# Optimization experiments

Measured on AMD Instinct MI355X. Metric: run time of the kernel, lower is better.

Reference implementation:

```python
import jax, jax.numpy as jnp
import numpy as np

N_HEAD, N_MIX, D_MODEL, D_K, D_V = 8, 2, 512, 64, 64
BN_EPS = 1e-5


def avg_pool_3x3_s2(x):
    # AvgPool2d(kernel=3, stride=2, pad=1, count_include_pad=False) on NCHW
    win = (1, 1, 3, 3)
    stride = (1, 1, 2, 2)
    pad = [(0, 0), (0, 0), (1, 1), (1, 1)]
    s = jax.lax.reduce_window(x, 0.0, jax.lax.add, win, stride, pad)
    ones = jnp.ones((1, 1, x.shape[2], x.shape[3]), x.dtype)
    cnt = jax.lax.reduce_window(ones, 0.0, jax.lax.add, win, stride, pad)
    return s / cnt


def conv1x1(x, w, b=None):
    # w: [out_c, in_c]; x: [B, in_c, H, W]
    y = jnp.einsum('oc,bchw->bohw', w, x)
    if b is not None:
        y = y + b[None, :, None, None]
    return y


def setup_inputs() -> dict:
    key = jax.random.key(0)
    ks = jax.random.split(key, 8)
    B, H, W = 2, 56, 56
    std_kq = np.sqrt(2.0 / (D_MODEL + D_K)).astype(np.float32)
    std_v = np.sqrt(2.0 / (D_MODEL + D_V)).astype(np.float32)
    std_mix = np.power(N_MIX, -0.5).astype(np.float32)
    return {
        'x': jax.random.normal(ks[0], (B, D_MODEL, H, W), jnp.float32),
        'w_qs': jax.random.normal(ks[1], (N_HEAD * D_K, D_MODEL), jnp.float32) * std_kq,
        'b_qs': jnp.zeros((N_HEAD * D_K,), jnp.float32),
        'w_vs': jax.random.normal(ks[2], (N_HEAD * D_V, D_MODEL), jnp.float32) * std_v,
        'b_vs': jnp.zeros((N_HEAD * D_V,), jnp.float32),
        'mix_w': jax.random.uniform(ks[3], (N_MIX, D_K), jnp.float32, -std_mix, std_mix),
        'w_out': jax.random.normal(ks[4], (D_MODEL, N_HEAD * D_V), jnp.float32) * 0.02,
        'bn_gamma': jnp.ones((D_MODEL,), jnp.float32),
        'bn_beta': jnp.zeros((D_MODEL,), jnp.float32),
    }


def reference(x, w_qs, b_qs, w_vs, b_vs, mix_w, w_out, bn_gamma, bn_beta):
    B, C, H, W = x.shape
    N = H * W
    m = N_MIX
    d = D_K // m  # per-mixture dim
    temperature = D_K ** 0.5

    px = avg_pool_3x3_s2(x)  # [B, C, H/2, W/2]
    N2 = px.shape[2] * px.shape[3]

    # conv_ks aliases conv_qs in the original (shared weights)
    qt = conv1x1(x, w_qs, b_qs).reshape(B * N_HEAD, D_K, N)
    kt = conv1x1(px, w_qs, b_qs).reshape(B * N_HEAD, D_K, N2)
    vt = conv1x1(px, w_vs, b_vs).reshape(B * N_HEAD, D_V, N2)

    # mixture weights pi: softmax over mixtures of weight @ mean_q
    bar_qt = qt.mean(axis=2)  # [B', D_K]
    pi = jax.nn.softmax(jnp.einsum('md,bd->bm', mix_w, bar_qt), axis=1)  # [B', m]

    q = qt.reshape(B * N_HEAD * m, d, N).transpose(0, 2, 1)  # [B'm, N, d]
    k2 = kt.reshape(B * N_HEAD * m, d, N2)  # [B'm, d, N2]

    attn = jnp.einsum('bnd,bdk->bnk', q, k2) / temperature  # [B'm, N, N2]
    attn = jax.nn.softmax(attn, axis=2)
    # dropout is identity in eval mode
    attn = (attn * pi.reshape(-1, 1, 1)).reshape(B * N_HEAD, m, N, N2).sum(1)

    out = jnp.einsum('bnk,bvk->bnv', attn, vt)  # [B', N, D_V]
    out = out.transpose(0, 2, 1).reshape(B, N_HEAD * D_V, H, W)
    out = conv1x1(out, w_out)  # no bias
    # BatchNorm2d in eval mode: running_mean=0, running_var=1
    inv = 1.0 / jnp.sqrt(jnp.float32(1.0 + BN_EPS))
    out = out * inv * bn_gamma[None, :, None, None] + bn_beta[None, :, None, None]
    return out + x
```

## Files before the change

### kernel.cpp

```cpp
#include <hip/hip_runtime.h>
#include <math.h>

typedef unsigned short u16;
typedef short bf16x8 __attribute__((ext_vector_type(8)));
typedef float f32x4 __attribute__((ext_vector_type(4)));

#define MFMA(a, b, c) __builtin_amdgcn_mfma_f32_16x16x32_bf16(a, b, c, 0, 0, 0)

#define SCALE_K 0.18033688011112043f

__device__ __forceinline__ float bf2f(u16 v) {
    union { float f; unsigned u; } x;
    x.u = ((unsigned)v) << 16;
    return x.f;
}
__device__ __forceinline__ u16 f2bf(float f) {
    union { float f; unsigned u; } x;
    x.f = f;
    unsigned r = x.u + 0x7FFF + ((x.u >> 16) & 1);
    return (u16)(r >> 16);
}

__global__ __launch_bounds__(256) void cvt_kernel(const float* __restrict__ s0,
                                                  const float* __restrict__ s1,
                                                  const float* __restrict__ s2,
                                                  u16* __restrict__ d0, u16* __restrict__ d1,
                                                  u16* __restrict__ d2) {
    int i = blockIdx.x * 256 + threadIdx.x;
    const float* s = (blockIdx.y == 0) ? s0 : ((blockIdx.y == 1) ? s1 : s2);
    u16* d = (blockIdx.y == 0) ? d0 : ((blockIdx.y == 1) ? d1 : d2);
    d[i] = f2bf(s[i]);
}

__global__ __launch_bounds__(256) void transpose_kernel(const float* __restrict__ x,
                                                        u16* __restrict__ xT) {
    __shared__ u16 tile[64][65];
    int b = blockIdx.z;
    int n0 = blockIdx.x * 64, c0 = blockIdx.y * 64;
    int j = threadIdx.x & 63, q = threadIdx.x >> 6;
    const float* xb = x + b * 512 * 3136;
#pragma unroll
    for (int it = 0; it < 16; ++it) {
        int r = q * 16 + it;
        tile[r][j] = f2bf(xb[(c0 + r) * 3136 + n0 + j]);
    }
    __syncthreads();
    u16* xTb = xT + b * 3136 * 512;
#pragma unroll
    for (int it = 0; it < 16; ++it) {
        int r = q * 16 + it;
        xTb[(n0 + r) * 512 + c0 + j] = tile[j][r];
    }
}

__global__ __launch_bounds__(256) void pool_kernel(const u16* __restrict__ xT,
                                                   u16* __restrict__ pxT) {
    int n2 = blockIdx.x;
    int b = blockIdx.y;
    int t = threadIdx.x;
    int i = n2 / 28, jj = n2 % 28;
    float s0 = 0.f, s1 = 0.f;
    int cnt = 0;
    const u16* xb = xT + b * 3136 * 512;
#pragma unroll
    for (int dr = 0; dr < 3; dr++) {
        int r = 2 * i - 1 + dr;
        if (r < 0 || r >= 56) continue;
#pragma unroll
        for (int dc = 0; dc < 3; dc++) {
            int cc = 2 * jj - 1 + dc;
            if (cc < 0 || cc >= 56) continue;
            const u16* row = xb + (r * 56 + cc) * 512;
            s0 += bf2f(row[t]);
            s1 += bf2f(row[t + 256]);
            cnt++;
        }
    }
    float invc = 1.0f / (float)cnt;
    u16* op = pxT + (b * 784 + n2) * 512;
    op[t] = f2bf(s0 * invc);
    op[t + 256] = f2bf(s1 * invc);
}

__device__ __forceinline__ void gemm_core(const u16* __restrict__ A, int lda, int M,
                                          const u16* __restrict__ BT, int ldb, int Ncol,
                                          int K, int row0, int col0, f32x4 acc[4][4]) {
    int lane = threadIdx.x & 63;
    int lr = lane & 15, lg = lane >> 4;
    int ar[4], bc[4];
#pragma unroll
    for (int i = 0; i < 4; i++) {
        int r = row0 + i * 16 + lr;
        ar[i] = (r < M) ? r : (M - 1);
    }
#pragma unroll
    for (int j = 0; j < 4; j++) {
        int cj = col0 + j * 16 + lr;
        bc[j] = (cj < Ncol) ? cj : (Ncol - 1);
    }
    for (int k = 0; k < K; k += 32) {
        int ko = k + lg * 8;
        bf16x8 af[4], bfr[4];
#pragma unroll
        for (int i = 0; i < 4; i++) af[i] = *(const bf16x8*)(A + ar[i] * lda + ko);
#pragma unroll
        for (int j = 0; j < 4; j++) bfr[j] = *(const bf16x8*)(BT + bc[j] * ldb + ko);
#pragma unroll
        for (int i = 0; i < 4; i++)
#pragma unroll
            for (int j = 0; j < 4; j++) acc[i][j] = MFMA(af[i], bfr[j], acc[i][j]);
    }
}

__global__ __launch_bounds__(256) void gemm_qk(const u16* __restrict__ xT,
                                               const u16* __restrict__ W,
                                               const float* __restrict__ bias,
                                               u16* __restrict__ out, int M, int Npad,
                                               float oscale) {
    int b = blockIdx.z;
    int w = threadIdx.x >> 6;
    int row0 = blockIdx.y * 128 + (w >> 1) * 64;
    int col0 = blockIdx.x * 128 + (w & 1) * 64;
    f32x4 acc[4][4];
#pragma unroll
    for (int i = 0; i < 4; i++)
#pragma unroll
        for (int j = 0; j < 4; j++) acc[i][j] = (f32x4){0.f, 0.f, 0.f, 0.f};
    gemm_core(xT + b * M * 512, 512, M, W, 512, 512, 512, row0, col0, acc);
    int lane = threadIdx.x & 63;
    int lr = lane & 15, lg = lane >> 4;
#pragma unroll
    for (int j = 0; j < 4; j++) {
        int oc = col0 + j * 16 + lr;
        float bs = bias[oc];
        int bh = b * 8 + (oc >> 6), dk = oc & 63;
        u16* op = out + (bh * Npad) * 64 + dk;
#pragma unroll
        for (int i = 0; i < 4; i++) {
#pragma unroll
            for (int r = 0; r < 4; r++) {
                int n = row0 + i * 16 + lg * 4 + r;
                if (n < M) op[n * 64] = f2bf((acc[i][j][r] + bs) * oscale);
                else if (n < Npad) op[n * 64] = 0;
            }
        }
    }
}

__global__ __launch_bounds__(256) void gemm_v(const u16* __restrict__ W,
                                              const u16* __restrict__ pxT,
                                              const float* __restrict__ bias,
                                              u16* __restrict__ vt) {
    int b = blockIdx.z;
    int w = threadIdx.x >> 6;
    int row0 = blockIdx.y * 128 + (w >> 1) * 64;
    int col0 = blockIdx.x * 128 + (w & 1) * 64;
    f32x4 acc[4][4];
#pragma unroll
    for (int i = 0; i < 4; i++)
#pragma unroll
        for (int j = 0; j < 4; j++) acc[i][j] = (f32x4){0.f, 0.f, 0.f, 0.f};
    gemm_core(W, 512, 512, pxT + b * 784 * 512, 512, 784, 512, row0, col0, acc);
    int lane = threadIdx.x & 63;
    int lr = lane & 15, lg = lane >> 4;
#pragma unroll
    for (int i = 0; i < 4; i++) {
#pragma unroll
        for (int r = 0; r < 4; r++) {
            int oc = row0 + i * 16 + lg * 4 + r;
            float bs = bias[oc];
            u16* vp = vt + ((b * 8 + (oc >> 6)) * 80 + (oc & 63)) * 800;
#pragma unroll
            for (int j = 0; j < 4; j++) {
                int n2 = col0 + j * 16 + lr;
                if (n2 < 784) vp[n2] = f2bf(acc[i][j][r] + bs);
                else if (n2 < 800) vp[n2] = 0;
            }
        }
    }
}

__global__ __launch_bounds__(256) void vpad_kernel(u16* __restrict__ vt) {
    int idx = blockIdx.x * 256 + threadIdx.x;
    int col = idx % 800;
    int row = (idx / 800) & 15;
    int bh = idx / (16 * 800);
    u16 v = (row == 0 && col < 784) ? (u16)0x3F80 : (u16)0;
    vt[(bh * 80 + 64 + row) * 800 + col] = v;
}

__global__ __launch_bounds__(256) void pi_stage1(const u16* __restrict__ qt,
                                                 float* __restrict__ part) {
    __shared__ float red[4][64];
    int chunk = blockIdx.x, bh = blockIdx.y;
    int t = threadIdx.x, dk = t & 63, seg = t >> 6;
    const u16* q = qt + (bh * 3136 + chunk * 112) * 64 + dk;
    float s = 0.f;
    for (int n = seg; n < 112; n += 4) s += bf2f(q[n * 64]);
    red[seg][dk] = s;
    __syncthreads();
    if (t < 64) part[(bh * 28 + chunk) * 64 + t] =
        red[0][t] + red[1][t] + red[2][t] + red[3][t];
}

__global__ __launch_bounds__(64) void pi_stage2(const float* __restrict__ part,
                                                const float* __restrict__ mix_w,
                                                float* __restrict__ pi) {
    int bh = blockIdx.x, lane = threadIdx.x;
    float bar = 0.f;
#pragma unroll
    for (int c = 0; c < 28; c++) bar += part[(bh * 28 + c) * 64 + lane];
    bar *= (1.0f / 3136.0f);
    float l0 = mix_w[lane] * bar;
    float l1 = mix_w[64 + lane] * bar;
#pragma unroll
    for (int d = 1; d < 64; d <<= 1) {
        l0 += __shfl_xor(l0, d);
        l1 += __shfl_xor(l1, d);
    }
    if (lane == 0) {
        float mx = fmaxf(l0, l1);
        float e0 = __expf(l0 - mx), e1 = __expf(l1 - mx);
        float inv = 1.0f / (e0 + e1);
        pi[bh * 2 + 0] = e0 * inv;
        pi[bh * 2 + 1] = e1 * inv;
    }
}

__global__ __launch_bounds__(256) void attn_kernel(const u16* __restrict__ qt,
                                                   const u16* __restrict__ kt,
                                                   const u16* __restrict__ vt,
                                                   const float* __restrict__ pi,
                                                   u16* __restrict__ ao) {
    __shared__ __attribute__((aligned(16))) u16 p_lds[4][2][16][40];
    int w = threadIdx.x >> 6, lane = threadIdx.x & 63;
    int lr = lane & 15, lg = lane >> 4;
    int bh = blockIdx.y;
    int qbase = (blockIdx.x * 4 + w) * 16;
    const u16* qp = qt + (bh * 3136 + qbase) * 64;
    const u16* kp = kt + bh * 800 * 64;
    const u16* vp = vt + bh * 80 * 800;

    bf16x8 qf[2];
    qf[0] = *(const bf16x8*)(qp + lr * 64 + lg * 8);
    qf[1] = *(const bf16x8*)(qp + lr * 64 + 32 + lg * 8);

    f32x4 O[2][4], Osum[2];
#pragma unroll
    for (int m = 0; m < 2; m++) {
#pragma unroll
        for (int t = 0; t < 4; t++) O[m][t] = (f32x4){0.f, 0.f, 0.f, 0.f};
        Osum[m] = (f32x4){0.f, 0.f, 0.f, 0.f};
    }

    for (int c = 0; c < 25; ++c) {
        int base = c * 32;
        bf16x8 vf[4], vfs;
#pragma unroll
        for (int t = 0; t < 4; t++)
            vf[t] = *(const bf16x8*)(vp + (t * 16 + lr) * 800 + base + lg * 8);
        vfs = *(const bf16x8*)(vp + (64 + lr) * 800 + base + lg * 8);
#pragma unroll
        for (int m = 0; m < 2; m++) {
            bf16x8 kf0 = *(const bf16x8*)(kp + (base + lr) * 64 + m * 32 + lg * 8);
            bf16x8 kf1 = *(const bf16x8*)(kp + (base + 16 + lr) * 64 + m * 32 + lg * 8);
            f32x4 s0 = MFMA(qf[m], kf0, ((f32x4){0.f, 0.f, 0.f, 0.f}));
            f32x4 s1 = MFMA(qf[m], kf1, ((f32x4){0.f, 0.f, 0.f, 0.f}));
#pragma unroll
            for (int r = 0; r < 4; r++) {
                float p0 = __builtin_amdgcn_exp2f(s0[r]);
                float p1 = __builtin_amdgcn_exp2f(s1[r]);
                unsigned u;
                asm("v_cvt_pk_bf16_f32 %0, %1, %2" : "=v"(u) : "v"(p0), "v"(p1));
                p_lds[w][m][lg * 4 + r][lr] = (u16)u;
                p_lds[w][m][lg * 4 + r][16 + lr] = (u16)(u >> 16);
            }
        }
#pragma unroll
        for (int m = 0; m < 2; m++) {
            bf16x8 pf = *(const bf16x8*)(&p_lds[w][m][lr][lg * 8]);
#pragma unroll
            for (int t = 0; t < 4; t++) O[m][t] = MFMA(pf, vf[t], O[m][t]);
            Osum[m] = MFMA(pf, vfs, Osum[m]);
        }
    }

    float pi0 = pi[bh * 2], pi1 = pi[bh * 2 + 1];
    float inv0[4], inv1[4];
#pragma unroll
    for (int r = 0; r < 4; r++) {
        float l0 = __shfl(Osum[0][r], lane & 48);
        float l1 = __shfl(Osum[1][r], lane & 48);
        inv0[r] = pi0 / l0;
        inv1[r] = pi1 / l1;
    }
    int b = bh >> 3, h = bh & 7;
    u16* aop = ao + ((b * 3136 + qbase) * 512) + h * 64;
#pragma unroll
    for (int t = 0; t < 4; t++) {
#pragma unroll
        for (int r = 0; r < 4; r++) {
            int n = lg * 4 + r;
            float v = inv0[r] * O[0][t][r] + inv1[r] * O[1][t][r];
            aop[n * 512 + t * 16 + lr] = f2bf(v);
        }
    }
}

__global__ __launch_bounds__(256) void gemm_out(const u16* __restrict__ W,
                                                const u16* __restrict__ aoT,
                                                const float* __restrict__ gamma,
                                                const float* __restrict__ beta,
                                                const float* __restrict__ xres,
                                                float* __restrict__ out) {
    int b = blockIdx.z;
    int w = threadIdx.x >> 6;
    int row0 = blockIdx.y * 128 + (w >> 1) * 64;
    int col0 = blockIdx.x * 128 + (w & 1) * 64;
    f32x4 acc[4][4];
#pragma unroll
    for (int i = 0; i < 4; i++)
#pragma unroll
        for (int j = 0; j < 4; j++) acc[i][j] = (f32x4){0.f, 0.f, 0.f, 0.f};
    gemm_core(W, 512, 512, aoT + b * 3136 * 512, 512, 3136, 512, row0, col0, acc);
    const float inv = 0.99999500003749969f;
    int lane = threadIdx.x & 63;
    int lr = lane & 15, lg = lane >> 4;
#pragma unroll
    for (int i = 0; i < 4; i++) {
#pragma unroll
        for (int r = 0; r < 4; r++) {
            int oc = row0 + i * 16 + lg * 4 + r;
            float g = gamma[oc] * inv;
            float bt = beta[oc];
            const float* xp = xres + (b * 512 + oc) * 3136;
            float* op = out + (b * 512 + oc) * 3136;
#pragma unroll
            for (int j = 0; j < 4; j++) {
                int n = col0 + j * 16 + lr;
                if (n < 3136) op[n] = acc[i][j][r] * g + bt + xp[n];
            }
        }
    }
}

extern "C" void kernel_launch(void* const* d_in, const int* in_sizes, int n_in,
                              void* d_out, int out_size, void* d_ws, size_t ws_size,
                              hipStream_t stream) {
    const float* x = (const float*)d_in[0];
    const float* w_qs = (const float*)d_in[1];
    const float* b_qs = (const float*)d_in[2];
    const float* w_vs = (const float*)d_in[3];
    const float* b_vs = (const float*)d_in[4];
    const float* mix_w = (const float*)d_in[5];
    const float* w_out = (const float*)d_in[6];
    const float* gamma = (const float*)d_in[7];
    const float* beta = (const float*)d_in[8];
    float* out = (float*)d_out;

    char* ws = (char*)d_ws;
    u16* xT = (u16*)(ws + 0);
    u16* ao = (u16*)(ws + 0);
    u16* pxT = (u16*)(ws + 6422528);
    u16* qt = (u16*)(ws + 8028160);
    u16* kt = (u16*)(ws + 14450688);
    u16* vt = (u16*)(ws + 16089088);
    u16* wq_b = (u16*)(ws + 18137088);
    u16* wv_b = (u16*)(ws + 18661376);
    u16* wo_b = (u16*)(ws + 19185664);
    float* pi = (float*)(ws + 19709952);
    float* part = (float*)(ws + 19710080);

    hipLaunchKernelGGL(cvt_kernel, dim3(1024, 3), dim3(256), 0, stream, w_qs, w_vs, w_out,
                       wq_b, wv_b, wo_b);
    hipLaunchKernelGGL(transpose_kernel, dim3(49, 8, 2), dim3(256), 0, stream, x, xT);
    hipLaunchKernelGGL(pool_kernel, dim3(784, 2), dim3(256), 0, stream, xT, pxT);
    hipLaunchKernelGGL(gemm_qk, dim3(4, 25, 2), dim3(256), 0, stream, xT, wq_b, b_qs, qt,
                       3136, 3136, 1.0f);
    hipLaunchKernelGGL(gemm_qk, dim3(4, 7, 2), dim3(256), 0, stream, pxT, wq_b, b_qs, kt,
                       784, 800, SCALE_K);
    hipLaunchKernelGGL(gemm_v, dim3(7, 4, 2), dim3(256), 0, stream, wv_b, pxT, b_vs, vt);
    hipLaunchKernelGGL(vpad_kernel, dim3(800), dim3(256), 0, stream, vt);
    hipLaunchKernelGGL(pi_stage1, dim3(28, 16), dim3(256), 0, stream, qt, part);
    hipLaunchKernelGGL(pi_stage2, dim3(16), dim3(64), 0, stream, part, mix_w, pi);
    hipLaunchKernelGGL(attn_kernel, dim3(49, 16), dim3(256), 0, stream, qt, kt, vt, pi, ao);
    hipLaunchKernelGGL(gemm_out, dim3(25, 4, 2), dim3(256), 0, stream, wo_b, ao, gamma,
                       beta, x, out);
}
```

Before: 228.6 us.

## Double-buffer K/V register loads in attention and interleave heads across blocks

The attention inner loop now prefetches the next chunk's K and V fragments into a second register set while the current chunk is computed, so global load latency is hidden behind MFMA and exp work. The grid is flattened to 1D with the head index in the low bits, so consecutive blocks cover different heads and scheduling and cache behaviour change. The extra buffers raise register pressure, which may lower occupancy.

```diff
diff --git a/kernel.cpp b/kernel.cpp
--- a/kernel.cpp
+++ b/kernel.cpp
@@ -235,8 +235,9 @@
     __shared__ __attribute__((aligned(16))) u16 p_lds[4][2][16][40];
     int w = threadIdx.x >> 6, lane = threadIdx.x & 63;
     int lr = lane & 15, lg = lane >> 4;
-    int bh = blockIdx.y;
-    int qbase = (blockIdx.x * 4 + w) * 16;
+    int bh = blockIdx.x & 15;
+    int xq = blockIdx.x >> 4;
+    int qbase = (xq * 4 + w) * 16;
     const u16* qp = qt + (bh * 3136 + qbase) * 64;
     const u16* kp = kt + bh * 800 * 64;
     const u16* vp = vt + bh * 80 * 800;
@@ -253,19 +254,24 @@
         Osum[m] = (f32x4){0.f, 0.f, 0.f, 0.f};
     }
 
-    for (int c = 0; c < 25; ++c) {
-        int base = c * 32;
-        bf16x8 vf[4], vfs;
+    auto loadV = [&](int base, bf16x8* vf, bf16x8& vfs) {
 #pragma unroll
         for (int t = 0; t < 4; t++)
             vf[t] = *(const bf16x8*)(vp + (t * 16 + lr) * 800 + base + lg * 8);
         vfs = *(const bf16x8*)(vp + (64 + lr) * 800 + base + lg * 8);
+    };
+    auto loadK = [&](int base, bf16x8 (*kf)[2]) {
 #pragma unroll
         for (int m = 0; m < 2; m++) {
-            bf16x8 kf0 = *(const bf16x8*)(kp + (base + lr) * 64 + m * 32 + lg * 8);
-            bf16x8 kf1 = *(const bf16x8*)(kp + (base + 16 + lr) * 64 + m * 32 + lg * 8);
-            f32x4 s0 = MFMA(qf[m], kf0, ((f32x4){0.f, 0.f, 0.f, 0.f}));
-            f32x4 s1 = MFMA(qf[m], kf1, ((f32x4){0.f, 0.f, 0.f, 0.f}));
+            kf[m][0] = *(const bf16x8*)(kp + (base + lr) * 64 + m * 32 + lg * 8);
+            kf[m][1] = *(const bf16x8*)(kp + (base + 16 + lr) * 64 + m * 32 + lg * 8);
+        }
+    };
+    auto compute = [&](bf16x8* vf, bf16x8& vfs, bf16x8 (*kf)[2]) {
+#pragma unroll
+        for (int m = 0; m < 2; m++) {
+            f32x4 s0 = MFMA(qf[m], kf[m][0], ((f32x4){0.f, 0.f, 0.f, 0.f}));
+            f32x4 s1 = MFMA(qf[m], kf[m][1], ((f32x4){0.f, 0.f, 0.f, 0.f}));
 #pragma unroll
             for (int r = 0; r < 4; r++) {
                 float p0 = __builtin_amdgcn_exp2f(s0[r]);
@@ -283,7 +289,21 @@
             for (int t = 0; t < 4; t++) O[m][t] = MFMA(pf, vf[t], O[m][t]);
             Osum[m] = MFMA(pf, vfs, Osum[m]);
         }
-    }
+    };
+
+    bf16x8 vfA[4], vfsA, kfA[2][2];
+    bf16x8 vfB[4], vfsB, kfB[2][2];
+    loadV(0, vfA, vfsA);
+    loadK(0, kfA);
+    for (int c = 0; c < 24; c += 2) {
+        loadV((c + 1) * 32, vfB, vfsB);
+        loadK((c + 1) * 32, kfB);
+        compute(vfA, vfsA, kfA);
+        loadV((c + 2) * 32, vfA, vfsA);
+        loadK((c + 2) * 32, kfA);
+        compute(vfB, vfsB, kfB);
+    }
+    compute(vfA, vfsA, kfA);
 
     float pi0 = pi[bh * 2], pi1 = pi[bh * 2 + 1];
     float inv0[4], inv1[4];
@@ -383,7 +403,7 @@
     hipLaunchKernelGGL(vpad_kernel, dim3(800), dim3(256), 0, stream, vt);
     hipLaunchKernelGGL(pi_stage1, dim3(28, 16), dim3(256), 0, stream, qt, part);
     hipLaunchKernelGGL(pi_stage2, dim3(16), dim3(64), 0, stream, part, mix_w, pi);
-    hipLaunchKernelGGL(attn_kernel, dim3(49, 16), dim3(256), 0, stream, qt, kt, vt, pi, ao);
+    hipLaunchKernelGGL(attn_kernel, dim3(784), dim3(256), 0, stream, qt, kt, vt, pi, ao);
     hipLaunchKernelGGL(gemm_out, dim3(25, 4, 2), dim3(256), 0, stream, wo_b, ao, gamma,
                        beta, x, out);
 }
```

Result: no change. 228.9 us (+0.1%).
